# Performance work log

Measured on AMD Instinct MI355X. Metric: run time of the kernel, lower is better.

The kernel has to match this reference:

```python
import jax, jax.numpy as jnp
import numpy as np

SEQ = 512
D_MODEL = 256
NUM_HEADS = 8


def setup_inputs() -> dict:
    key = jax.random.key(0)
    k1, k2, k3, k4, k5, k6 = jax.random.split(key, 6)
    d = D_MODEL
    scale = 1.0 / np.sqrt(d)
    q = jax.random.normal(k1, (SEQ, d), dtype=jnp.float32)
    k = jax.random.normal(k2, (SEQ, d), dtype=jnp.float32)
    v = jax.random.normal(k3, (SEQ, d), dtype=jnp.float32)
    # eqx.nn.Linear weights have shape [out_features, in_features]
    Wq = jax.random.normal(k4, (d, d), dtype=jnp.float32) * scale
    Wk_hyper = jax.random.normal(k5, (d * d, d), dtype=jnp.float32) * scale
    Wv_hyper = jax.random.normal(k6, (d * d, d), dtype=jnp.float32) * scale
    # causal mask: every query row attends to >=1 key, matching softmax(where=mask)
    mask = jnp.tril(jnp.ones((SEQ, SEQ), dtype=bool))
    return {"q": q, "k": k, "v": v, "Wq": Wq, "Wk_hyper": Wk_hyper,
            "Wv_hyper": Wv_hyper, "mask": mask}


def reference(q, k, v, Wq, Wk_hyper, Wv_hyper, mask):
    s, d = q.shape
    n = NUM_HEADS
    dh = d // n
    # q projection (Linear, no bias): y = x @ W.T
    qp = q @ Wq.T                                   # [s, d]
    # hypernetwork per-query projection matrices P[i, j_out, k_in]
    Pk = (qp @ Wk_hyper.T).reshape(s, d, d)         # [s, d, d]
    Pv = (qp @ Wv_hyper.T).reshape(s, d, d)
    # per-query K/V cubes: K[i, l, j] = sum_k Pk[i, j, k] * k[l, k]
    Kc = jnp.einsum('sjk,lk->slj', Pk, k)           # [s, s, d]
    Vc = jnp.einsum('sjk,lk->slj', Pv, v)           # [s, s, d]
    # split heads
    qh = qp.reshape(s, n, dh)                       # [s, n, dh]
    Kh = Kc.reshape(s, s, n, dh)                    # [s_q, s_kv, n, dh]
    Vh = Vc.reshape(s, s, n, dh)
    # NOTE: original scales by 1/sqrt(kv_seq) (k.shape[0]), not sqrt(head_dim)
    logits = jnp.einsum('snd,stnd->nst', qh, Kh) / jnp.sqrt(jnp.float32(s))
    logits = jnp.where(mask[None, :, :], logits, -jnp.inf)
    probs = jax.nn.softmax(logits, axis=-1)         # [n, s_q, s_kv]
    out = jnp.einsum('nst,stnd->snd', probs, Vh)    # [s, n, dh]
    return out.reshape(s, d)
```

## Files before the change

kernel.cpp:

```cpp
#include <hip/hip_runtime.h>
#include <hip/hip_bf16.h>
#include <math.h>

#define SEQ 512
#define DM  256
#define NH  8

typedef __attribute__((ext_vector_type(4))) float  f32x4;
typedef __attribute__((ext_vector_type(8))) __bf16 bf16x8;
typedef __attribute__((ext_vector_type(8))) short  s16x8;

__device__ __forceinline__ unsigned short f2bf(float f) {
  unsigned int u = __builtin_bit_cast(unsigned int, f);
  u += 0x7fffu + ((u >> 16) & 1u);
  return (unsigned short)(u >> 16);
}
__device__ __forceinline__ float bf2f(unsigned short h) {
  unsigned int u = ((unsigned int)h) << 16;
  return __builtin_bit_cast(float, u);
}
__device__ __forceinline__ void gll16(const void* g, void* ldsbase) {
  __builtin_amdgcn_global_load_lds((const __attribute__((address_space(1))) void*)g,
                                   (__attribute__((address_space(3))) void*)ldsbase,
                                   16, 0, 0);
}

__global__ __launch_bounds__(256) void kconv(const float* __restrict__ src,
                                             unsigned short* __restrict__ dst) {
  size_t base = ((size_t)blockIdx.x * 256 + threadIdx.x) * 32;
  #pragma unroll
  for (int u = 0; u < 4; u++) {
    float4 a = *(const float4*)(src + base + u * 8);
    float4 b = *(const float4*)(src + base + u * 8 + 4);
    s16x8 o;
    o[0]=f2bf(a.x); o[1]=f2bf(a.y); o[2]=f2bf(a.z); o[3]=f2bf(a.w);
    o[4]=f2bf(b.x); o[5]=f2bf(b.y); o[6]=f2bf(b.z); o[7]=f2bf(b.w);
    *(s16x8*)(dst + base + u * 8) = o;
  }
}

__global__ __launch_bounds__(256) void k0_convert(const float* __restrict__ kin,
                                                  const float* __restrict__ vin,
                                                  unsigned short* __restrict__ kbf,
                                                  unsigned short* __restrict__ vT) {
  __shared__ unsigned short tl[64][72];
  int b = blockIdx.x, t = threadIdx.x;
  if (b < 32) {
    int base = b * 4096 + t * 16;
    float4 a0 = *(const float4*)(kin + base);
    float4 a1 = *(const float4*)(kin + base + 4);
    float4 a2 = *(const float4*)(kin + base + 8);
    float4 a3 = *(const float4*)(kin + base + 12);
    s16x8 o0, o1;
    o0[0]=f2bf(a0.x); o0[1]=f2bf(a0.y); o0[2]=f2bf(a0.z); o0[3]=f2bf(a0.w);
    o0[4]=f2bf(a1.x); o0[5]=f2bf(a1.y); o0[6]=f2bf(a1.z); o0[7]=f2bf(a1.w);
    o1[0]=f2bf(a2.x); o1[1]=f2bf(a2.y); o1[2]=f2bf(a2.z); o1[3]=f2bf(a2.w);
    o1[4]=f2bf(a3.x); o1[5]=f2bf(a3.y); o1[6]=f2bf(a3.z); o1[7]=f2bf(a3.w);
    *(s16x8*)(kbf + base)     = o0;
    *(s16x8*)(kbf + base + 8) = o1;
  } else {
    int tb = b - 32;
    int i0 = (tb >> 2) * 64;
    int m0 = (tb & 3) * 64;
    int r = t >> 2, cq = t & 3;
    #pragma unroll
    for (int u = 0; u < 4; u++) {
      float4 x = *(const float4*)(vin + (size_t)(i0 + r) * DM + m0 + cq * 16 + u * 4);
      tl[cq*16 + u*4 + 0][r] = f2bf(x.x);
      tl[cq*16 + u*4 + 1][r] = f2bf(x.y);
      tl[cq*16 + u*4 + 2][r] = f2bf(x.z);
      tl[cq*16 + u*4 + 3][r] = f2bf(x.w);
    }
    __syncthreads();
    int mm = t >> 2;
    s16x8 w0, w1;
    #pragma unroll
    for (int e = 0; e < 8; e++) { w0[e] = tl[mm][cq*16 + e]; w1[e] = tl[mm][cq*16 + 8 + e]; }
    *(s16x8*)(vT + (size_t)(m0 + mm) * SEQ + i0 + cq * 16)     = w0;
    *(s16x8*)(vT + (size_t)(m0 + mm) * SEQ + i0 + cq * 16 + 8) = w1;
  }
}

__global__ __launch_bounds__(256) void k1_qproj(const float* __restrict__ q,
                                                const float* __restrict__ Wq,
                                                float* __restrict__ qpf) {
  __shared__ __align__(16) float qrow[DM];
  int i = blockIdx.x, t = threadIdx.x;
  if (t < 64) *(float4*)&qrow[t*4] = *(const float4*)(q + (size_t)i * DM + t * 4);
  __syncthreads();
  int w = t >> 6, lane = t & 63;
  for (int jj = 0; jj < 64; jj++) {
    int j = w * 64 + jj;
    float4 wv = *(const float4*)(Wq + (size_t)j * DM + lane * 4);
    float s = wv.x*qrow[lane*4] + wv.y*qrow[lane*4+1] + wv.z*qrow[lane*4+2] + wv.w*qrow[lane*4+3];
    #pragma unroll
    for (int off = 32; off; off >>= 1) s += __shfl_xor(s, off);
    if (lane == 0) qpf[(size_t)i*DM + j] = s;
  }
}

__global__ __launch_bounds__(256) void ka_gemm(const unsigned short* __restrict__ Wkb,
                                               const float* __restrict__ qpf,
                                               float* __restrict__ af) {
  __shared__ __align__(16) unsigned short lA[128 * 72];
  __shared__ __align__(16) unsigned short lB[128 * 64];
  int bid = blockIdx.x;
  int lid = (bid & 7) * 64 + (bid >> 3);
  int mtile = lid & 3, ntile = (lid >> 2) & 1, head = (lid >> 3) & 7, kchunk = lid >> 6;
  int m0 = mtile * 128, n0 = ntile * 128;
  int t = threadIdx.x, w = t >> 6, lane = t & 63;
  int wr = w >> 1, wc = w & 1;
  f32x4 acc[4][4] = {};

  for (int ks = 0; ks < 16; ks++) {
    int kt = kchunk * 1024 + ks * 64;
    int jcol = head * 32 + (kt >> 8);
    int mbase = kt & 255;
    __syncthreads();
    {
      const unsigned short* Bbase = Wkb + ((size_t)jcol * 256 + n0) * 256 + mbase;
      #pragma unroll
      for (int it = 0; it < 4; it++) {
        int r0 = (w * 4 + it) * 8 + (lane >> 3);
        int cbyte = ((lane & 7) * 16) ^ ((r0 & 7) << 4);
        gll16((const char*)(Bbase + (size_t)r0 * 256) + cbyte,
              (char*)lB + (w * 4 + it) * 1024);
      }
    }
    #pragma unroll
    for (int rep = 0; rep < 4; rep++) {
      int sc = rep * 256 + t;
      int row = sc >> 3, c8 = sc & 7;
      int i = m0 + row;
      float scal = qpf[(size_t)i * 256 + jcol];
      const float* src = qpf + (size_t)i * 256 + mbase + c8 * 8;
      float4 u0 = *(const float4*)src, u1 = *(const float4*)(src + 4);
      s16x8 o;
      o[0]=f2bf(scal*u0.x); o[1]=f2bf(scal*u0.y); o[2]=f2bf(scal*u0.z); o[3]=f2bf(scal*u0.w);
      o[4]=f2bf(scal*u1.x); o[5]=f2bf(scal*u1.y); o[6]=f2bf(scal*u1.z); o[7]=f2bf(scal*u1.w);
      *(s16x8*)&lA[row * 72 + c8 * 8] = o;
    }
    __syncthreads();
    #pragma unroll
    for (int kk = 0; kk < 2; kk++) {
      int r = lane & 15, kc = kk * 32 + (lane >> 4) * 8;
      bf16x8 afr[4], bfr[4];
      #pragma unroll
      for (int mf = 0; mf < 4; mf++) afr[mf] = *(const bf16x8*)&lA[(wr*64 + mf*16 + r) * 72 + kc];
      #pragma unroll
      for (int nf = 0; nf < 4; nf++) {
        int row = wc*64 + nf*16 + r;
        int cb = (kc * 2) ^ ((row & 7) << 4);
        bfr[nf] = *(const bf16x8*)((const char*)lB + row * 128 + cb);
      }
      #pragma unroll
      for (int mf = 0; mf < 4; mf++)
        #pragma unroll
        for (int nf = 0; nf < 4; nf++)
          acc[mf][nf] = __builtin_amdgcn_mfma_f32_16x16x32_bf16(afr[mf], bfr[nf], acc[mf][nf], 0, 0, 0);
    }
  }
  int cr = (lane >> 4) * 4, cc = lane & 15;
  #pragma unroll
  for (int mf = 0; mf < 4; mf++)
    #pragma unroll
    for (int nf = 0; nf < 4; nf++)
      #pragma unroll
      for (int qq = 0; qq < 4; qq++) {
        int i   = m0 + wr*64 + mf*16 + cr + qq;
        int col = n0 + wc*64 + nf*16 + cc;
        atomicAdd(&af[((size_t)head * SEQ + i) * 256 + col], acc[mf][nf][qq]);
      }
}

__global__ __launch_bounds__(256) void ko_gemm(const unsigned short* __restrict__ Wvb,
                                               const float* __restrict__ qpf,
                                               const unsigned short* __restrict__ wbf,
                                               float* __restrict__ out) {
  __shared__ __align__(16) unsigned short lA[128 * 72];
  __shared__ __align__(16) unsigned short lB[32 * 64];
  int bid = blockIdx.x;
  int lid = (bid & 7) * 64 + (bid >> 3);
  int mtile = lid & 3, head = (lid >> 2) & 7, kchunk = lid >> 5;
  int m0 = mtile * 128;
  int t = threadIdx.x, w = t >> 6, lane = t & 63;
  f32x4 acc[2][2] = {};

  for (int ks = 0; ks < 64; ks++) {
    int kt = kchunk * 4096 + ks * 64;
    int kdim = kt >> 8;
    int mbase = kt & 255;
    __syncthreads();
    {
      int r0 = w * 8 + (lane >> 3);
      int cbyte = ((lane & 7) * 16) ^ ((r0 & 7) << 4);
      const unsigned short* Bb = Wvb + (((size_t)head * 32 + r0) * 256 + kdim) * 256 + mbase;
      gll16((const char*)Bb + cbyte, (char*)lB + w * 1024);
    }
    #pragma unroll
    for (int rep = 0; rep < 4; rep++) {
      int sc = rep * 256 + t;
      int row = sc >> 3, c8 = sc & 7;
      int i = m0 + row;
      float scal = bf2f(wbf[((size_t)head * SEQ + i) * 256 + kdim]);
      const float* src = qpf + (size_t)i * 256 + mbase + c8 * 8;
      float4 u0 = *(const float4*)src, u1 = *(const float4*)(src + 4);
      s16x8 o;
      o[0]=f2bf(scal*u0.x); o[1]=f2bf(scal*u0.y); o[2]=f2bf(scal*u0.z); o[3]=f2bf(scal*u0.w);
      o[4]=f2bf(scal*u1.x); o[5]=f2bf(scal*u1.y); o[6]=f2bf(scal*u1.z); o[7]=f2bf(scal*u1.w);
      *(s16x8*)&lA[row * 72 + c8 * 8] = o;
    }
    __syncthreads();
    #pragma unroll
    for (int kk = 0; kk < 2; kk++) {
      int r = lane & 15, kc = kk * 32 + (lane >> 4) * 8;
      bf16x8 afr[2], bfr[2];
      #pragma unroll
      for (int mf = 0; mf < 2; mf++) afr[mf] = *(const bf16x8*)&lA[(w*32 + mf*16 + r) * 72 + kc];
      #pragma unroll
      for (int nf = 0; nf < 2; nf++) {
        int row = nf*16 + r;
        int cb = (kc * 2) ^ ((row & 7) << 4);
        bfr[nf] = *(const bf16x8*)((const char*)lB + row * 128 + cb);
      }
      #pragma unroll
      for (int mf = 0; mf < 2; mf++)
        #pragma unroll
        for (int nf = 0; nf < 2; nf++)
          acc[mf][nf] = __builtin_amdgcn_mfma_f32_16x16x32_bf16(afr[mf], bfr[nf], acc[mf][nf], 0, 0, 0);
    }
  }
  int cr = (lane >> 4) * 4, cc = lane & 15;
  #pragma unroll
  for (int mf = 0; mf < 2; mf++)
    #pragma unroll
    for (int nf = 0; nf < 2; nf++)
      #pragma unroll
      for (int qq = 0; qq < 4; qq++) {
        int i   = m0 + w*32 + mf*16 + cr + qq;
        int col = head * 32 + nf*16 + cc;
        atomicAdd(&out[(size_t)i * 256 + col], acc[mf][nf][qq]);
      }
}

template<int CONVA, int OUTBF>
__global__ __launch_bounds__(256) void gemm_small(const void* __restrict__ Ap,
                                                  const unsigned short* __restrict__ B,
                                                  void* __restrict__ Cp,
                                                  int M, int N, int K, int nMtiles) {
  __shared__ __align__(16) unsigned short lA[64 * 72];
  __shared__ __align__(16) unsigned short lB[64 * 72];
  int bid = blockIdx.x;
  int mtile = bid % nMtiles, ntile = bid / nMtiles;
  int m0 = mtile * 64, n0 = ntile * 64;
  int t = threadIdx.x, w = t >> 6, lane = t & 63;
  int wr = w >> 1, wc = w & 1;
  f32x4 acc[2][2] = {};
  for (int kt = 0; kt < K; kt += 64) {
    __syncthreads();
    #pragma unroll
    for (int rep = 0; rep < 2; rep++) {
      int sc = rep * 256 + t;
      int row = sc >> 3, c8 = sc & 7;
      if (CONVA) {
        const float* src = (const float*)Ap + (size_t)(m0 + row) * K + kt + c8 * 8;
        float4 u0 = *(const float4*)src, u1 = *(const float4*)(src + 4);
        s16x8 o;
        o[0]=f2bf(u0.x); o[1]=f2bf(u0.y); o[2]=f2bf(u0.z); o[3]=f2bf(u0.w);
        o[4]=f2bf(u1.x); o[5]=f2bf(u1.y); o[6]=f2bf(u1.z); o[7]=f2bf(u1.w);
        *(s16x8*)&lA[row * 72 + c8 * 8] = o;
      } else {
        *(s16x8*)&lA[row * 72 + c8 * 8] =
            *(const s16x8*)((const unsigned short*)Ap + (size_t)(m0 + row) * K + kt + c8 * 8);
      }
      *(s16x8*)&lB[row * 72 + c8 * 8] = *(const s16x8*)(B + (size_t)(n0 + row) * K + kt + c8 * 8);
    }
    __syncthreads();
    #pragma unroll
    for (int kk = 0; kk < 2; kk++) {
      int r = lane & 15, kc = kk * 32 + (lane >> 4) * 8;
      bf16x8 afr[2], bfr[2];
      #pragma unroll
      for (int mf = 0; mf < 2; mf++) afr[mf] = *(const bf16x8*)&lA[(wr*32 + mf*16 + r) * 72 + kc];
      #pragma unroll
      for (int nf = 0; nf < 2; nf++) bfr[nf] = *(const bf16x8*)&lB[(wc*32 + nf*16 + r) * 72 + kc];
      #pragma unroll
      for (int mf = 0; mf < 2; mf++)
        #pragma unroll
        for (int nf = 0; nf < 2; nf++)
          acc[mf][nf] = __builtin_amdgcn_mfma_f32_16x16x32_bf16(afr[mf], bfr[nf], acc[mf][nf], 0, 0, 0);
    }
  }
  int cr = (lane >> 4) * 4, cc = lane & 15;
  #pragma unroll
  for (int mf = 0; mf < 2; mf++)
    #pragma unroll
    for (int nf = 0; nf < 2; nf++)
      #pragma unroll
      for (int qq = 0; qq < 4; qq++) {
        int row = m0 + wr*32 + mf*16 + cr + qq;
        int col = n0 + wc*32 + nf*16 + cc;
        float vv = acc[mf][nf][qq];
        if (OUTBF) ((unsigned short*)Cp)[(size_t)row * N + col] = f2bf(vv);
        else       ((float*)Cp)[(size_t)row * N + col] = vv;
      }
}

__global__ __launch_bounds__(256) void k4b_softmax(const float* __restrict__ logits,
                                                   unsigned short* __restrict__ probs) {
  __shared__ float red[4];
  __shared__ float red2[4];
  int m = blockIdx.x, t = threadIdx.x;
  int i = m & (SEQ - 1);
  const float scale = 0.04419417382415922f;
  const float NEG = -1e30f;
  float v0 = (t       <= i) ? logits[(size_t)m * SEQ + t      ] * scale : NEG;
  float v1 = (t + 256 <= i) ? logits[(size_t)m * SEQ + t + 256] * scale : NEG;
  float mx = fmaxf(v0, v1);
  #pragma unroll
  for (int off = 32; off; off >>= 1) mx = fmaxf(mx, __shfl_xor(mx, off));
  int w = t >> 6, lane = t & 63;
  if (lane == 0) red[w] = mx;
  __syncthreads();
  mx = fmaxf(fmaxf(red[0], red[1]), fmaxf(red[2], red[3]));
  float e0 = (t       <= i) ? __expf(v0 - mx) : 0.f;
  float e1 = (t + 256 <= i) ? __expf(v1 - mx) : 0.f;
  float s = e0 + e1;
  #pragma unroll
  for (int off = 32; off; off >>= 1) s += __shfl_xor(s, off);
  if (lane == 0) red2[w] = s;
  __syncthreads();
  s = red2[0] + red2[1] + red2[2] + red2[3];
  float inv = 1.f / s;
  probs[(size_t)m * SEQ + t]       = f2bf(e0 * inv);
  probs[(size_t)m * SEQ + t + 256] = f2bf(e1 * inv);
}

extern "C" void kernel_launch(void* const* d_in, const int* in_sizes, int n_in,
                              void* d_out, int out_size, void* d_ws, size_t ws_size,
                              hipStream_t stream) {
  (void)in_sizes; (void)n_in; (void)out_size; (void)ws_size;
  const float* q  = (const float*)d_in[0];
  const float* k  = (const float*)d_in[1];
  const float* v  = (const float*)d_in[2];
  const float* Wq = (const float*)d_in[3];
  const float* Wk = (const float*)d_in[4];
  const float* Wv = (const float*)d_in[5];
  float* out = (float*)d_out;

  char* ws = (char*)d_ws;
  size_t off = 0;
  auto alloc = [&](size_t bytes) -> void* {
    void* p = ws + off; off += (bytes + 255) & ~(size_t)255; return p;
  };
  float*          qpf    = (float*)         alloc((size_t)SEQ * DM * 4);
  unsigned short* kbf    = (unsigned short*)alloc((size_t)SEQ * DM * 2);
  unsigned short* vT     = (unsigned short*)alloc((size_t)DM * SEQ * 2);
  unsigned short* Wkb    = (unsigned short*)alloc((size_t)DM * DM * DM * 2);
  unsigned short* Wvb    = (unsigned short*)alloc((size_t)DM * DM * DM * 2);
  float*          af     = (float*)         alloc((size_t)NH * SEQ * DM * 4);
  float*          logits = (float*)         alloc((size_t)NH * SEQ * SEQ * 4);
  unsigned short* probs  = (unsigned short*)alloc((size_t)NH * SEQ * SEQ * 2);
  unsigned short* wbf    = (unsigned short*)alloc((size_t)NH * SEQ * DM * 2);

  hipMemsetAsync(af, 0, (size_t)NH * SEQ * DM * 4, stream);
  hipMemsetAsync(out, 0, (size_t)SEQ * DM * 4, stream);

  kconv<<<2048, 256, 0, stream>>>(Wk, Wkb);
  kconv<<<2048, 256, 0, stream>>>(Wv, Wvb);
  k0_convert<<<64, 256, 0, stream>>>(k, v, kbf, vT);
  k1_qproj<<<SEQ, 256, 0, stream>>>(q, Wq, qpf);
  ka_gemm<<<512, 256, 0, stream>>>(Wkb, qpf, af);
  gemm_small<1,0><<<512, 256, 0, stream>>>((const void*)af, kbf, (void*)logits, NH*SEQ, SEQ, DM, 64);
  k4b_softmax<<<NH*SEQ, 256, 0, stream>>>(logits, probs);
  gemm_small<0,1><<<256, 256, 0, stream>>>((const void*)probs, vT, (void*)wbf, NH*SEQ, DM, SEQ, 64);
  ko_gemm<<<512, 256, 0, stream>>>(Wvb, qpf, wbf, out);
}
```

Before: 378.6 us.

## Fuse fp32-to-bf16 hyper-weight conversion into restructured hypernetwork GEMMs

Drops the two standalone kernels that converted the 64M-element Wk and Wv hypernetwork weights to bf16. The K and V GEMMs now read the fp32 weights directly and convert them while staging into LDS. Both GEMMs are restructured so each block computes a per-j qp@W_j^T product and then scales it by qp[i,j] (or by wbf in the output GEMM) in registers. The intent is to remove a full write and re-read of 256MB of bf16 weight copies, at the cost of more fp32 traffic per GEMM, no async global-to-LDS loads and no LDS swizzle.

```diff
diff --git a/kernel.cpp b/kernel.cpp
--- a/kernel.cpp
+++ b/kernel.cpp
@@ -10,6 +10,10 @@
 typedef __attribute__((ext_vector_type(8))) __bf16 bf16x8;
 typedef __attribute__((ext_vector_type(8))) short  s16x8;
 
+__device__ __forceinline__ short fb(float x) {
+  __bf16 h = (__bf16)x;
+  return __builtin_bit_cast(short, h);
+}
 __device__ __forceinline__ unsigned short f2bf(float f) {
   unsigned int u = __builtin_bit_cast(unsigned int, f);
   u += 0x7fffu + ((u >> 16) & 1u);
@@ -19,24 +23,11 @@
   unsigned int u = ((unsigned int)h) << 16;
   return __builtin_bit_cast(float, u);
 }
-__device__ __forceinline__ void gll16(const void* g, void* ldsbase) {
-  __builtin_amdgcn_global_load_lds((const __attribute__((address_space(1))) void*)g,
-                                   (__attribute__((address_space(3))) void*)ldsbase,
-                                   16, 0, 0);
-}
-
-__global__ __launch_bounds__(256) void kconv(const float* __restrict__ src,
-                                             unsigned short* __restrict__ dst) {
-  size_t base = ((size_t)blockIdx.x * 256 + threadIdx.x) * 32;
-  #pragma unroll
-  for (int u = 0; u < 4; u++) {
-    float4 a = *(const float4*)(src + base + u * 8);
-    float4 b = *(const float4*)(src + base + u * 8 + 4);
-    s16x8 o;
-    o[0]=f2bf(a.x); o[1]=f2bf(a.y); o[2]=f2bf(a.z); o[3]=f2bf(a.w);
-    o[4]=f2bf(b.x); o[5]=f2bf(b.y); o[6]=f2bf(b.z); o[7]=f2bf(b.w);
-    *(s16x8*)(dst + base + u * 8) = o;
-  }
+__device__ __forceinline__ s16x8 cvt8(float4 a, float4 b) {
+  s16x8 o;
+  o[0]=fb(a.x); o[1]=fb(a.y); o[2]=fb(a.z); o[3]=fb(a.w);
+  o[4]=fb(b.x); o[5]=fb(b.y); o[6]=fb(b.z); o[7]=fb(b.w);
+  return o;
 }
 
 __global__ __launch_bounds__(256) void k0_convert(const float* __restrict__ kin,
@@ -51,13 +42,8 @@
     float4 a1 = *(const float4*)(kin + base + 4);
     float4 a2 = *(const float4*)(kin + base + 8);
     float4 a3 = *(const float4*)(kin + base + 12);
-    s16x8 o0, o1;
-    o0[0]=f2bf(a0.x); o0[1]=f2bf(a0.y); o0[2]=f2bf(a0.z); o0[3]=f2bf(a0.w);
-    o0[4]=f2bf(a1.x); o0[5]=f2bf(a1.y); o0[6]=f2bf(a1.z); o0[7]=f2bf(a1.w);
-    o1[0]=f2bf(a2.x); o1[1]=f2bf(a2.y); o1[2]=f2bf(a2.z); o1[3]=f2bf(a2.w);
-    o1[4]=f2bf(a3.x); o1[5]=f2bf(a3.y); o1[6]=f2bf(a3.z); o1[7]=f2bf(a3.w);
-    *(s16x8*)(kbf + base)     = o0;
-    *(s16x8*)(kbf + base + 8) = o1;
+    *(s16x8*)(kbf + base)     = cvt8(a0, a1);
+    *(s16x8*)(kbf + base + 8) = cvt8(a2, a3);
   } else {
     int tb = b - 32;
     int i0 = (tb >> 2) * 64;
@@ -66,10 +52,10 @@
     #pragma unroll
     for (int u = 0; u < 4; u++) {
       float4 x = *(const float4*)(vin + (size_t)(i0 + r) * DM + m0 + cq * 16 + u * 4);
-      tl[cq*16 + u*4 + 0][r] = f2bf(x.x);
-      tl[cq*16 + u*4 + 1][r] = f2bf(x.y);
-      tl[cq*16 + u*4 + 2][r] = f2bf(x.z);
-      tl[cq*16 + u*4 + 3][r] = f2bf(x.w);
+      tl[cq*16 + u*4 + 0][r] = (unsigned short)fb(x.x);
+      tl[cq*16 + u*4 + 1][r] = (unsigned short)fb(x.y);
+      tl[cq*16 + u*4 + 2][r] = (unsigned short)fb(x.z);
+      tl[cq*16 + u*4 + 3][r] = (unsigned short)fb(x.w);
     }
     __syncthreads();
     int mm = t >> 2;
@@ -99,148 +85,161 @@
   }
 }
 
-__global__ __launch_bounds__(256) void ka_gemm(const unsigned short* __restrict__ Wkb,
-                                               const float* __restrict__ qpf,
-                                               float* __restrict__ af) {
-  __shared__ __align__(16) unsigned short lA[128 * 72];
-  __shared__ __align__(16) unsigned short lB[128 * 64];
+__global__ __launch_bounds__(256) void ka3(const float* __restrict__ Wk,
+                                           const float* __restrict__ qpf,
+                                           float* __restrict__ af) {
+  __shared__ __align__(16) unsigned short lA[64 * 76];
+  __shared__ __align__(16) unsigned short lB[256 * 76];
+  __shared__ __align__(16) float lqs[64 * 4];
   int bid = blockIdx.x;
   int lid = (bid & 7) * 64 + (bid >> 3);
-  int mtile = lid & 3, ntile = (lid >> 2) & 1, head = (lid >> 3) & 7, kchunk = lid >> 6;
-  int m0 = mtile * 128, n0 = ntile * 128;
-  int t = threadIdx.x, w = t >> 6, lane = t & 63;
-  int wr = w >> 1, wc = w & 1;
+  int head = lid >> 6, jsplit = (lid >> 3) & 7, itile = lid & 7;
+  int m0 = itile * 64;
+  int t = threadIdx.x, wc = t >> 6, lane = t & 63;
+  int r = lane & 15, hi = lane >> 4;
+
+  { int row = t >> 2, jl = t & 3;
+    lqs[row*4 + jl] = qpf[(size_t)(m0+row)*DM + head*32 + jsplit*4 + jl]; }
+
   f32x4 acc[4][4] = {};
-
-  for (int ks = 0; ks < 16; ks++) {
-    int kt = kchunk * 1024 + ks * 64;
-    int jcol = head * 32 + (kt >> 8);
-    int mbase = kt & 255;
-    __syncthreads();
-    {
-      const unsigned short* Bbase = Wkb + ((size_t)jcol * 256 + n0) * 256 + mbase;
-      #pragma unroll
-      for (int it = 0; it < 4; it++) {
-        int r0 = (w * 4 + it) * 8 + (lane >> 3);
-        int cbyte = ((lane & 7) * 16) ^ ((r0 & 7) << 4);
-        gll16((const char*)(Bbase + (size_t)r0 * 256) + cbyte,
-              (char*)lB + (w * 4 + it) * 1024);
-      }
-    }
-    #pragma unroll
-    for (int rep = 0; rep < 4; rep++) {
-      int sc = rep * 256 + t;
-      int row = sc >> 3, c8 = sc & 7;
-      int i = m0 + row;
-      float scal = qpf[(size_t)i * 256 + jcol];
-      const float* src = qpf + (size_t)i * 256 + mbase + c8 * 8;
-      float4 u0 = *(const float4*)src, u1 = *(const float4*)(src + 4);
-      s16x8 o;
-      o[0]=f2bf(scal*u0.x); o[1]=f2bf(scal*u0.y); o[2]=f2bf(scal*u0.z); o[3]=f2bf(scal*u0.w);
-      o[4]=f2bf(scal*u1.x); o[5]=f2bf(scal*u1.y); o[6]=f2bf(scal*u1.z); o[7]=f2bf(scal*u1.w);
-      *(s16x8*)&lA[row * 72 + c8 * 8] = o;
-    }
-    __syncthreads();
-    #pragma unroll
-    for (int kk = 0; kk < 2; kk++) {
-      int r = lane & 15, kc = kk * 32 + (lane >> 4) * 8;
-      bf16x8 afr[4], bfr[4];
-      #pragma unroll
-      for (int mf = 0; mf < 4; mf++) afr[mf] = *(const bf16x8*)&lA[(wr*64 + mf*16 + r) * 72 + kc];
-      #pragma unroll
-      for (int nf = 0; nf < 4; nf++) {
-        int row = wc*64 + nf*16 + r;
-        int cb = (kc * 2) ^ ((row & 7) << 4);
-        bfr[nf] = *(const bf16x8*)((const char*)lB + row * 128 + cb);
-      }
-      #pragma unroll
-      for (int mf = 0; mf < 4; mf++)
-        #pragma unroll
-        for (int nf = 0; nf < 4; nf++)
-          acc[mf][nf] = __builtin_amdgcn_mfma_f32_16x16x32_bf16(afr[mf], bfr[nf], acc[mf][nf], 0, 0, 0);
-    }
-  }
-  int cr = (lane >> 4) * 4, cc = lane & 15;
+  int srow = t >> 2, sc16 = (t & 3) * 16;
+
+  for (int jj = 0; jj < 4; jj++) {
+    int jcol = head*32 + jsplit*4 + jj;
+    const float* Bbase = Wk + (size_t)jcol * 65536;
+    f32x4 tmp[4][4] = {};
+    for (int kt = 0; kt < 4; kt++) {
+      __syncthreads();
+      {
+        const float* src = qpf + (size_t)(m0+srow)*DM + kt*64 + sc16;
+        float4 x0 = *(const float4*)src,     x1 = *(const float4*)(src+4);
+        float4 x2 = *(const float4*)(src+8), x3 = *(const float4*)(src+12);
+        *(s16x8*)&lA[srow*76 + sc16]     = cvt8(x0, x1);
+        *(s16x8*)&lA[srow*76 + sc16 + 8] = cvt8(x2, x3);
+      }
+      #pragma unroll
+      for (int p = 0; p < 4; p++) {
+        int row = p*64 + srow;
+        const float* src = Bbase + (size_t)row*256 + kt*64 + sc16;
+        float4 x0 = *(const float4*)src,     x1 = *(const float4*)(src+4);
+        float4 x2 = *(const float4*)(src+8), x3 = *(const float4*)(src+12);
+        *(s16x8*)&lB[row*76 + sc16]     = cvt8(x0, x1);
+        *(s16x8*)&lB[row*76 + sc16 + 8] = cvt8(x2, x3);
+      }
+      __syncthreads();
+      #pragma unroll
+      for (int kk = 0; kk < 2; kk++) {
+        int kc = kk*32 + hi*8;
+        bf16x8 afr[4], bfr[4];
+        #pragma unroll
+        for (int mf = 0; mf < 4; mf++) afr[mf] = *(const bf16x8*)&lA[(mf*16 + r)*76 + kc];
+        #pragma unroll
+        for (int nf = 0; nf < 4; nf++) bfr[nf] = *(const bf16x8*)&lB[(wc*64 + nf*16 + r)*76 + kc];
+        #pragma unroll
+        for (int mf = 0; mf < 4; mf++)
+          #pragma unroll
+          for (int nf = 0; nf < 4; nf++)
+            tmp[mf][nf] = __builtin_amdgcn_mfma_f32_16x16x32_bf16(afr[mf], bfr[nf], tmp[mf][nf], 0, 0, 0);
+      }
+    }
+    #pragma unroll
+    for (int mf = 0; mf < 4; mf++)
+      #pragma unroll
+      for (int qq = 0; qq < 4; qq++) {
+        float sv = lqs[(mf*16 + hi*4 + qq)*4 + jj];
+        #pragma unroll
+        for (int nf = 0; nf < 4; nf++) acc[mf][nf][qq] += sv * tmp[mf][nf][qq];
+      }
+  }
   #pragma unroll
   for (int mf = 0; mf < 4; mf++)
     #pragma unroll
     for (int nf = 0; nf < 4; nf++)
       #pragma unroll
       for (int qq = 0; qq < 4; qq++) {
-        int i   = m0 + wr*64 + mf*16 + cr + qq;
-        int col = n0 + wc*64 + nf*16 + cc;
-        atomicAdd(&af[((size_t)head * SEQ + i) * 256 + col], acc[mf][nf][qq]);
-      }
-}
-
-__global__ __launch_bounds__(256) void ko_gemm(const unsigned short* __restrict__ Wvb,
-                                               const float* __restrict__ qpf,
-                                               const unsigned short* __restrict__ wbf,
-                                               float* __restrict__ out) {
-  __shared__ __align__(16) unsigned short lA[128 * 72];
-  __shared__ __align__(16) unsigned short lB[32 * 64];
+        int row = m0 + mf*16 + hi*4 + qq;
+        int col = wc*64 + nf*16 + r;
+        atomicAdd(&af[((size_t)head * SEQ + row) * DM + col], acc[mf][nf][qq]);
+      }
+}
+
+__global__ __launch_bounds__(256) void ko3(const float* __restrict__ Wv,
+                                           const float* __restrict__ qpf,
+                                           const unsigned short* __restrict__ wbf,
+                                           float* __restrict__ out) {
+  __shared__ __align__(16) unsigned short lA[32 * 76];
+  __shared__ __align__(16) unsigned short lB[256 * 76];
+  __shared__ __align__(16) unsigned short lw[32 * 264];
   int bid = blockIdx.x;
-  int lid = (bid & 7) * 64 + (bid >> 3);
-  int mtile = lid & 3, head = (lid >> 2) & 7, kchunk = lid >> 5;
-  int m0 = mtile * 128;
-  int t = threadIdx.x, w = t >> 6, lane = t & 63;
-  f32x4 acc[2][2] = {};
-
-  for (int ks = 0; ks < 64; ks++) {
-    int kt = kchunk * 4096 + ks * 64;
-    int kdim = kt >> 8;
-    int mbase = kt & 255;
-    __syncthreads();
-    {
-      int r0 = w * 8 + (lane >> 3);
-      int cbyte = ((lane & 7) * 16) ^ ((r0 & 7) << 4);
-      const unsigned short* Bb = Wvb + (((size_t)head * 32 + r0) * 256 + kdim) * 256 + mbase;
-      gll16((const char*)Bb + cbyte, (char*)lB + w * 1024);
-    }
-    #pragma unroll
-    for (int rep = 0; rep < 4; rep++) {
-      int sc = rep * 256 + t;
-      int row = sc >> 3, c8 = sc & 7;
-      int i = m0 + row;
-      float scal = bf2f(wbf[((size_t)head * SEQ + i) * 256 + kdim]);
-      const float* src = qpf + (size_t)i * 256 + mbase + c8 * 8;
-      float4 u0 = *(const float4*)src, u1 = *(const float4*)(src + 4);
-      s16x8 o;
-      o[0]=f2bf(scal*u0.x); o[1]=f2bf(scal*u0.y); o[2]=f2bf(scal*u0.z); o[3]=f2bf(scal*u0.w);
-      o[4]=f2bf(scal*u1.x); o[5]=f2bf(scal*u1.y); o[6]=f2bf(scal*u1.z); o[7]=f2bf(scal*u1.w);
-      *(s16x8*)&lA[row * 72 + c8 * 8] = o;
-    }
-    __syncthreads();
-    #pragma unroll
-    for (int kk = 0; kk < 2; kk++) {
-      int r = lane & 15, kc = kk * 32 + (lane >> 4) * 8;
-      bf16x8 afr[2], bfr[2];
-      #pragma unroll
-      for (int mf = 0; mf < 2; mf++) afr[mf] = *(const bf16x8*)&lA[(w*32 + mf*16 + r) * 72 + kc];
-      #pragma unroll
-      for (int nf = 0; nf < 2; nf++) {
-        int row = nf*16 + r;
-        int cb = (kc * 2) ^ ((row & 7) << 4);
-        bfr[nf] = *(const bf16x8*)((const char*)lB + row * 128 + cb);
-      }
-      #pragma unroll
-      for (int mf = 0; mf < 2; mf++)
-        #pragma unroll
-        for (int nf = 0; nf < 2; nf++)
-          acc[mf][nf] = __builtin_amdgcn_mfma_f32_16x16x32_bf16(afr[mf], bfr[nf], acc[mf][nf], 0, 0, 0);
-    }
-  }
-  int cr = (lane >> 4) * 4, cc = lane & 15;
-  #pragma unroll
-  for (int mf = 0; mf < 2; mf++)
-    #pragma unroll
-    for (int nf = 0; nf < 2; nf++)
+  int lid = (bid & 7) * 128 + (bid >> 3);
+  int head = lid >> 7, jsplit = (lid >> 4) & 7, itile = lid & 15;
+  int m0 = itile * 32;
+  int t = threadIdx.x, wc = t >> 6, lane = t & 63;
+  int r = lane & 15, hi = lane >> 4;
+
+  {
+    int row = t >> 3, c32 = (t & 7) * 32;
+    const unsigned short* sw = wbf + ((size_t)head * SEQ + m0 + row) * DM + c32;
+    #pragma unroll
+    for (int u = 0; u < 4; u++)
+      *(s16x8*)&lw[row*264 + c32 + u*8] = *(const s16x8*)(sw + u*8);
+  }
+
+  int srow = t >> 2, sc16 = (t & 3) * 16;
+  int arow = t >> 3, ac8 = (t & 7) * 8;
+
+  for (int jj = 0; jj < 4; jj++) {
+    int jcol = head*32 + jsplit*4 + jj;
+    const float* Bbase = Wv + (size_t)jcol * 65536;
+    f32x4 tmp[2][4] = {};
+    for (int kt = 0; kt < 4; kt++) {
+      __syncthreads();
+      {
+        const float* src = qpf + (size_t)(m0+arow)*DM + kt*64 + ac8;
+        float4 x0 = *(const float4*)src, x1 = *(const float4*)(src+4);
+        *(s16x8*)&lA[arow*76 + ac8] = cvt8(x0, x1);
+      }
+      #pragma unroll
+      for (int p = 0; p < 4; p++) {
+        int row = p*64 + srow;
+        const float* src = Bbase + (size_t)row*256 + kt*64 + sc16;
+        float4 x0 = *(const float4*)src,     x1 = *(const float4*)(src+4);
+        float4 x2 = *(const float4*)(src+8), x3 = *(const float4*)(src+12);
+        *(s16x8*)&lB[row*76 + sc16]     = cvt8(x0, x1);
+        *(s16x8*)&lB[row*76 + sc16 + 8] = cvt8(x2, x3);
+      }
+      __syncthreads();
+      #pragma unroll
+      for (int kk = 0; kk < 2; kk++) {
+        int kc = kk*32 + hi*8;
+        bf16x8 afr[2], bfr[4];
+        #pragma unroll
+        for (int mf = 0; mf < 2; mf++) afr[mf] = *(const bf16x8*)&lA[(mf*16 + r)*76 + kc];
+        #pragma unroll
+        for (int nf = 0; nf < 4; nf++) bfr[nf] = *(const bf16x8*)&lB[(wc*64 + nf*16 + r)*76 + kc];
+        #pragma unroll
+        for (int mf = 0; mf < 2; mf++)
+          #pragma unroll
+          for (int nf = 0; nf < 4; nf++)
+            tmp[mf][nf] = __builtin_amdgcn_mfma_f32_16x16x32_bf16(afr[mf], bfr[nf], tmp[mf][nf], 0, 0, 0);
+      }
+    }
+    #pragma unroll
+    for (int mf = 0; mf < 2; mf++)
       #pragma unroll
       for (int qq = 0; qq < 4; qq++) {
-        int i   = m0 + w*32 + mf*16 + cr + qq;
-        int col = head * 32 + nf*16 + cc;
-        atomicAdd(&out[(size_t)i * 256 + col], acc[mf][nf][qq]);
-      }
+        int rloc = mf*16 + hi*4 + qq;
+        float pp = 0.f;
+        #pragma unroll
+        for (int nf = 0; nf < 4; nf++)
+          pp += tmp[mf][nf][qq] * bf2f(lw[rloc*264 + wc*64 + nf*16 + r]);
+        pp += __shfl_xor(pp, 1);
+        pp += __shfl_xor(pp, 2);
+        pp += __shfl_xor(pp, 4);
+        pp += __shfl_xor(pp, 8);
+        if (r == 0) atomicAdd(&out[(size_t)(m0 + rloc) * DM + jcol], pp);
+      }
+  }
 }
 
 template<int CONVA, int OUTBF>
@@ -254,7 +253,7 @@
   int mtile = bid % nMtiles, ntile = bid / nMtiles;
   int m0 = mtile * 64, n0 = ntile * 64;
   int t = threadIdx.x, w = t >> 6, lane = t & 63;
-  int wr = w >> 1, wc = w & 1;
+  int wr = w >> 1, wcc = w & 1;
   f32x4 acc[2][2] = {};
   for (int kt = 0; kt < K; kt += 64) {
     __syncthreads();
@@ -265,10 +264,7 @@
       if (CONVA) {
         const float* src = (const float*)Ap + (size_t)(m0 + row) * K + kt + c8 * 8;
         float4 u0 = *(const float4*)src, u1 = *(const float4*)(src + 4);
-        s16x8 o;
-        o[0]=f2bf(u0.x); o[1]=f2bf(u0.y); o[2]=f2bf(u0.z); o[3]=f2bf(u0.w);
-        o[4]=f2bf(u1.x); o[5]=f2bf(u1.y); o[6]=f2bf(u1.z); o[7]=f2bf(u1.w);
-        *(s16x8*)&lA[row * 72 + c8 * 8] = o;
+        *(s16x8*)&lA[row * 72 + c8 * 8] = cvt8(u0, u1);
       } else {
         *(s16x8*)&lA[row * 72 + c8 * 8] =
             *(const s16x8*)((const unsigned short*)Ap + (size_t)(m0 + row) * K + kt + c8 * 8);
@@ -283,7 +279,7 @@
       #pragma unroll
       for (int mf = 0; mf < 2; mf++) afr[mf] = *(const bf16x8*)&lA[(wr*32 + mf*16 + r) * 72 + kc];
       #pragma unroll
-      for (int nf = 0; nf < 2; nf++) bfr[nf] = *(const bf16x8*)&lB[(wc*32 + nf*16 + r) * 72 + kc];
+      for (int nf = 0; nf < 2; nf++) bfr[nf] = *(const bf16x8*)&lB[(wcc*32 + nf*16 + r) * 72 + kc];
       #pragma unroll
       for (int mf = 0; mf < 2; mf++)
         #pragma unroll
@@ -299,7 +295,7 @@
       #pragma unroll
       for (int qq = 0; qq < 4; qq++) {
         int row = m0 + wr*32 + mf*16 + cr + qq;
-        int col = n0 + wc*32 + nf*16 + cc;
+        int col = n0 + wcc*32 + nf*16 + cc;
         float vv = acc[mf][nf][qq];
         if (OUTBF) ((unsigned short*)Cp)[(size_t)row * N + col] = f2bf(vv);
         else       ((float*)Cp)[(size_t)row * N + col] = vv;
@@ -356,8 +352,6 @@
   float*          qpf    = (float*)         alloc((size_t)SEQ * DM * 4);
   unsigned short* kbf    = (unsigned short*)alloc((size_t)SEQ * DM * 2);
   unsigned short* vT     = (unsigned short*)alloc((size_t)DM * SEQ * 2);
-  unsigned short* Wkb    = (unsigned short*)alloc((size_t)DM * DM * DM * 2);
-  unsigned short* Wvb    = (unsigned short*)alloc((size_t)DM * DM * DM * 2);
   float*          af     = (float*)         alloc((size_t)NH * SEQ * DM * 4);
   float*          logits = (float*)         alloc((size_t)NH * SEQ * SEQ * 4);
   unsigned short* probs  = (unsigned short*)alloc((size_t)NH * SEQ * SEQ * 2);
@@ -366,13 +360,11 @@
   hipMemsetAsync(af, 0, (size_t)NH * SEQ * DM * 4, stream);
   hipMemsetAsync(out, 0, (size_t)SEQ * DM * 4, stream);
 
-  kconv<<<2048, 256, 0, stream>>>(Wk, Wkb);
-  kconv<<<2048, 256, 0, stream>>>(Wv, Wvb);
   k0_convert<<<64, 256, 0, stream>>>(k, v, kbf, vT);
   k1_qproj<<<SEQ, 256, 0, stream>>>(q, Wq, qpf);
-  ka_gemm<<<512, 256, 0, stream>>>(Wkb, qpf, af);
+  ka3<<<512, 256, 0, stream>>>(Wk, qpf, af);
   gemm_small<1,0><<<512, 256, 0, stream>>>((const void*)af, kbf, (void*)logits, NH*SEQ, SEQ, DM, 64);
   k4b_softmax<<<NH*SEQ, 256, 0, stream>>>(logits, probs);
   gemm_small<0,1><<<256, 256, 0, stream>>>((const void*)probs, vT, (void*)wbf, NH*SEQ, DM, SEQ, 64);
-  ko_gemm<<<512, 256, 0, stream>>>(Wvb, qpf, wbf, out);
-}
+  ko3<<<1024, 256, 0, stream>>>(Wv, qpf, wbf, out);
+}
```

New measurement: 430.2 us. 1.14x slower.
